# Performance work log

Measured on AMD Instinct MI355X. Metric: run time of the kernel, lower is better.

The kernel has to match this reference:

```python
import jax, jax.numpy as jnp
import numpy as np
from jax import lax

STRIDES = (4, 8, 16, 32, 64)
SIZES = (32, 64, 128, 256, 512)
RATIOS = (0.5, 1.0, 2.0)
IMG_H, IMG_W = 1024, 1024
PRE_NMS = 1000
POST_NMS = 1000
NMS_THRESH = 0.7
BBOX_CLIP = float(np.log(1000.0 / 16.0))
NEG_INF = -1e9


def _cell_anchors(size):
    a = []
    for r in RATIOS:
        w = size * np.sqrt(1.0 / r)
        h = size * np.sqrt(r)
        a.append([-w / 2.0, -h / 2.0, w / 2.0, h / 2.0])
    return np.array(a, np.float32)  # [A,4]


def _level_anchors(H, W, stride, size):
    cell = _cell_anchors(size)  # [A,4]
    ys = np.arange(H, dtype=np.float32) * stride
    xs = np.arange(W, dtype=np.float32) * stride
    yy, xx = np.meshgrid(ys, xs, indexing='ij')  # row-major (H,W)
    shifts = np.stack([xx, yy, xx, yy], axis=-1).reshape(-1, 1, 4)
    return jnp.asarray((shifts + cell[None]).reshape(-1, 4))  # [(H*W*A),4] in (H,W,A) order


def conv2d(x, w, b, pad):
    y = lax.conv_general_dilated(x, w, (1, 1), pad,
                                 dimension_numbers=('NCHW', 'OIHW', 'NCHW'))
    return y + b[None, :, None, None]


def decode(deltas, anchors):
    widths = anchors[:, 2] - anchors[:, 0] + 1.0
    heights = anchors[:, 3] - anchors[:, 1] + 1.0
    ctr_x = anchors[:, 0] + 0.5 * widths
    ctr_y = anchors[:, 1] + 0.5 * heights
    dx, dy = deltas[..., 0], deltas[..., 1]
    dw = jnp.minimum(deltas[..., 2], BBOX_CLIP)
    dh = jnp.minimum(deltas[..., 3], BBOX_CLIP)
    pcx = dx * widths + ctr_x
    pcy = dy * heights + ctr_y
    pw = jnp.exp(dw) * widths
    ph = jnp.exp(dh) * heights
    return jnp.stack([pcx - 0.5 * pw, pcy - 0.5 * ph,
                      pcx + 0.5 * pw - 1.0, pcy + 0.5 * ph - 1.0], axis=-1)


def iou_matrix(boxes):
    area = (boxes[:, 2] - boxes[:, 0]) * (boxes[:, 3] - boxes[:, 1])
    lt = jnp.maximum(boxes[:, None, :2], boxes[None, :, :2])
    rb = jnp.minimum(boxes[:, None, 2:], boxes[None, :, 2:])
    wh = jnp.maximum(rb - lt, 0.0)
    inter = wh[..., 0] * wh[..., 1]
    return inter / (area[:, None] + area[None, :] - inter + 1e-9)


def nms_keep(boxes):
    # boxes [N,4] already sorted by score desc; greedy NMS -> bool keep mask
    N = boxes.shape[0]
    iou = iou_matrix(boxes)

    def body(keep, i):
        row = jnp.take(iou, i, axis=0) > NMS_THRESH
        row = row.at[i].set(False)
        keep = jnp.where(keep[i], keep & ~row, keep)
        return keep, None

    keep, _ = lax.scan(body, jnp.ones((N,), bool), jnp.arange(N))
    return keep


def _forward(feats, conv_w, conv_b, cls_w, cls_b, bbox_w, bbox_b):
    level_boxes, level_scores = [], []
    for lvl, feat in enumerate(feats):
        B, _, H, W = feat.shape
        t = jax.nn.relu(conv2d(feat, conv_w, conv_b, 'SAME'))
        logits = conv2d(t, cls_w, cls_b, 'VALID')    # [B,A,H,W]
        breg = conv2d(t, bbox_w, bbox_b, 'VALID')    # [B,4A,H,W]
        A = logits.shape[1]
        scores = jnp.transpose(logits, (0, 2, 3, 1)).reshape(B, -1)            # (H,W,A)
        deltas = breg.reshape(B, A, 4, H, W).transpose(0, 3, 4, 1, 2).reshape(B, -1, 4)
        anchors = _level_anchors(H, W, STRIDES[lvl], SIZES[lvl])
        boxes = decode(deltas, anchors)  # [B,N,4]
        boxes = jnp.stack([jnp.clip(boxes[..., 0], 0.0, IMG_W - 1.0),
                           jnp.clip(boxes[..., 1], 0.0, IMG_H - 1.0),
                           jnp.clip(boxes[..., 2], 0.0, IMG_W - 1.0),
                           jnp.clip(boxes[..., 3], 0.0, IMG_H - 1.0)], axis=-1)
        k = min(PRE_NMS, scores.shape[1])
        top_s, idx = lax.top_k(scores, k)                                   # [B,k]
        top_b = jnp.take_along_axis(boxes, idx[..., None], axis=1)          # [B,k,4]
        keep = jax.vmap(nms_keep)(top_b)                                    # [B,k] bool
        level_scores.append(jnp.where(keep, top_s, NEG_INF))
        level_boxes.append(top_b)
    all_s = jnp.concatenate(level_scores, axis=1)
    all_b = jnp.concatenate(level_boxes, axis=1)
    fs, fi = lax.top_k(all_s, POST_NMS)                                     # [B,POST]
    fb = jnp.take_along_axis(all_b, fi[..., None], axis=1)                  # [B,POST,4]
    return jnp.concatenate([fb, fs[..., None]], axis=-1)                    # [B,POST,5]


def setup_inputs() -> dict:
    key = jax.random.key(0)
    ks = jax.random.split(key, 8)
    C = 256
    feats = {
        'feat0': jax.random.normal(ks[0], (2, C, 256, 256), jnp.float32),
        'feat1': jax.random.normal(ks[1], (2, C, 128, 128), jnp.float32),
        'feat2': jax.random.normal(ks[2], (2, C, 64, 64), jnp.float32),
        'feat3': jax.random.normal(ks[3], (2, C, 32, 32), jnp.float32),
        'feat4': jax.random.normal(ks[4], (2, C, 16, 16), jnp.float32),
    }
    params = {
        'conv_w': jax.random.normal(ks[5], (C, C, 3, 3), jnp.float32) * 0.01,
        'conv_b': jnp.zeros((C,), jnp.float32),
        'cls_w': jax.random.normal(ks[6], (3, C, 1, 1), jnp.float32) * 0.01,
        'cls_b': jnp.zeros((3,), jnp.float32),
        'bbox_w': jax.random.normal(ks[7], (12, C, 1, 1), jnp.float32) * 0.01,
        'bbox_b': jnp.zeros((12,), jnp.float32),
    }
    return {**feats, **params}


def reference(feat0, feat1, feat2, feat3, feat4, conv_w, conv_b, cls_w, cls_b, bbox_w, bbox_b):
    return _forward([feat0, feat1, feat2, feat3, feat4],
                    conv_w, conv_b, cls_w, cls_b, bbox_w, bbox_b)
```

## Files before the change

### kernel.cpp

```cpp
#include <hip/hip_runtime.h>
#include <cmath>


#define NTOT_PER_IMG 261888
#define ATOT_PER_IMG 4768

__constant__ int c_NLVL[5] = {196608, 49152, 12288, 3072, 768};
__constant__ int c_KLVL[5] = {1000, 1000, 1000, 1000, 768};
__constant__ int c_LOFF[5] = {0, 196608, 245760, 258048, 261120};
__constant__ int c_AOFF[5] = {0, 1000, 2000, 3000, 4000};

struct Anch { float cx1[3]; float cy1[3]; };
struct ConvCfg { Anch an[5]; };

__device__ __forceinline__ void ldsBarrier() {
  asm volatile("s_waitcnt lgkmcnt(0)" ::: "memory");
  __builtin_amdgcn_s_barrier();
  asm volatile("" ::: "memory");
}

__global__ __launch_bounds__(256) void wtrans(const float* __restrict__ Wsrc,
                                              float* __restrict__ Wt) {
  __shared__ float T[16][17];
  int k0 = blockIdx.x * 16;
  int o0 = blockIdx.y * 16;
  int i = threadIdx.x >> 4, j = threadIdx.x & 15;
  T[i][j] = Wsrc[(size_t)(o0 + i) * 2304 + (k0 + j)];
  __syncthreads();
  Wt[(size_t)(k0 + i) * 256 + (o0 + j)] = T[j][i];
}

__global__ __launch_bounds__(256, 2) void conv_gemm(
    const float* __restrict__ f0, const float* __restrict__ f1,
    const float* __restrict__ f2, const float* __restrict__ f3,
    const float* __restrict__ f4, const float* __restrict__ Wt,
    const float* __restrict__ convb, const float* __restrict__ clsw,
    const float* __restrict__ clsb, const float* __restrict__ bboxw,
    const float* __restrict__ bboxb, float* __restrict__ scoresOut,
    float4* __restrict__ boxesOut, ConvCfg cfg) {
  __shared__ __align__(16) float s_mem[5424];
  __shared__ float s_Red2[272];
  float* const s_w = s_mem;
  float* const s_x = s_mem + 4608;
  float* const s_tl = s_mem;

  int b = blockIdx.x;
  const float* feat;
  int lvl, img, tile, H, logW, stride, lvlOff;
  if (b < 2048) {
    lvl = 0; feat = f0; H = 256; logW = 8; stride = 4; lvlOff = 0;
    img = b >> 10; tile = b & 1023;
  } else if (b < 2560) {
    lvl = 1; feat = f1; H = 128; logW = 7; stride = 8; lvlOff = 196608;
    int r = b - 2048; img = r >> 8; tile = r & 255;
  } else if (b < 2688) {
    lvl = 2; feat = f2; H = 64; logW = 6; stride = 16; lvlOff = 245760;
    int r = b - 2560; img = r >> 6; tile = r & 63;
  } else if (b < 2720) {
    lvl = 3; feat = f3; H = 32; logW = 5; stride = 32; lvlOff = 258048;
    int r = b - 2688; img = r >> 4; tile = r & 15;
  } else {
    lvl = 4; feat = f4; H = 16; logW = 4; stride = 64; lvlOff = 261120;
    int r = b - 2720; img = r >> 2; tile = r & 3;
  }
  const int W = H, HW = H * W;
  const int p0 = tile * 64;
  const float* fimg = feat + (size_t)img * 256 * HW;

  const int log2nc = (logW < 6) ? logW : 6;
  const int ncols = 1 << log2nc;
  const int R = 64 >> log2nc;
  const int py0 = p0 >> logW;
  const int c_start = p0 & (W - 1);
  const int WIN = ncols + 2;
  const int NX = (R + 2) * WIN;

  const int tid = threadIdx.x;
  const int oc0 = (tid >> 3) * 8;
  const int pxg = tid & 7;
  const int px0 = pxg * 8;
  const int trow = px0 >> log2nc;
  const int tcol0 = px0 & (ncols - 1);

  int goffX = -1, loffX = -1;
  if (tid < NX) {
    int lr = tid / WIN;
    int lc = tid - lr * WIN;
    int sy = py0 - 1 + lr;
    int sx = c_start - 1 + lc;
    loffX = lr * 68 + lc;
    if (sy >= 0 && sy < H && sx >= 0 && sx < W) goffX = sy * W + sx;
  }

  float acc[8][8];
#pragma unroll
  for (int i = 0; i < 8; i++)
#pragma unroll
    for (int p = 0; p < 8; p++) acc[i][p] = 0.f;

  {
    const float4* wg = (const float4*)(Wt);
    float4* wl = (float4*)(s_w);
    wl[tid] = wg[tid];
    wl[tid + 256] = wg[tid + 256];
    if (tid < 64) wl[tid + 512] = wg[tid + 512];
    if (loffX >= 0) s_x[loffX] = (goffX >= 0) ? fimg[goffX] : 0.f;
  }
  ldsBarrier();

#pragma unroll 1
  for (int ic = 0; ic < 256; ic++) {
    const float* wb = s_w + (ic & 1) * 2304;
    const float* xb = s_x + (ic & 1) * 408;
    float* wn = s_w + ((ic + 1) & 1) * 2304;
    float* xn = s_x + ((ic + 1) & 1) * 408;

    float4 pw0, pw1, pw2;
    float pxv;
    if (ic < 255) {
      const float4* wg = (const float4*)(Wt + (size_t)(ic + 1) * 2304);
      pw0 = wg[tid];
      pw1 = wg[tid + 256];
      if (tid < 64) pw2 = wg[tid + 512];
      const float* fnext = fimg + (size_t)(ic + 1) * HW;
      pxv = (goffX >= 0) ? fnext[goffX] : 0.f;
    }

#pragma unroll
    for (int ky = 0; ky < 3; ky++) {
      const float* xr = xb + (trow + ky) * 68 + tcol0;
      float4 xA = *(const float4*)(xr);
      float4 xB = *(const float4*)(xr + 4);
      float2 xC = *(const float2*)(xr + 8);
      float xw[10] = {xA.x, xA.y, xA.z, xA.w,
                      xB.x, xB.y, xB.z, xB.w, xC.x, xC.y};
#pragma unroll
      for (int kx = 0; kx < 3; kx++) {
        const float* wr = wb + (ky * 3 + kx) * 256 + oc0;
        float4 wa = *(const float4*)(wr);
        float4 wc = *(const float4*)(wr + 4);
        float wv[8] = {wa.x, wa.y, wa.z, wa.w, wc.x, wc.y, wc.z, wc.w};
#pragma unroll
        for (int i = 0; i < 8; i++)
#pragma unroll
          for (int p = 0; p < 8; p++)
            acc[i][p] = __builtin_fmaf(wv[i], xw[p + kx], acc[i][p]);
      }
    }

    if (ic < 255) {
      float4* wl = (float4*)(wn);
      wl[tid] = pw0;
      wl[tid + 256] = pw1;
      if (tid < 64) wl[tid + 512] = pw2;
      if (loffX >= 0) xn[loffX] = pxv;
    }
    ldsBarrier();
  }

  float cb[8];
#pragma unroll
  for (int i = 0; i < 8; i++) cb[i] = convb[oc0 + i];

  const Anch an = cfg.an[lvl];
  const float BCLIP = (float)4.135166556742356;
  const size_t obase = (size_t)img * NTOT_PER_IMG + lvlOff;

#pragma unroll 1
  for (int r = 0; r < 4; r++) {
    if ((pxg >> 1) == r) {
      int pl = px0 - 16 * r;
#pragma unroll
      for (int p = 0; p < 8; p++) {
        float4 v0 = make_float4(fmaxf(acc[0][p] + cb[0], 0.f),
                                fmaxf(acc[1][p] + cb[1], 0.f),
                                fmaxf(acc[2][p] + cb[2], 0.f),
                                fmaxf(acc[3][p] + cb[3], 0.f));
        float4 v1 = make_float4(fmaxf(acc[4][p] + cb[4], 0.f),
                                fmaxf(acc[5][p] + cb[5], 0.f),
                                fmaxf(acc[6][p] + cb[6], 0.f),
                                fmaxf(acc[7][p] + cb[7], 0.f));
        *(float4*)(s_tl + (pl + p) * 256 + oc0) = v0;
        *(float4*)(s_tl + (pl + p) * 256 + oc0 + 4) = v1;
      }
    }
    __syncthreads();

    if (tid < 240) {
      int px = tid / 15, c = tid - px * 15;
      const float* wr0 = (c < 3) ? (clsw + c * 256) : (bboxw + (c - 3) * 256);
      float bb = (c < 3) ? clsb[c] : bboxb[c - 3];
      const float* trow2 = &s_tl[px * 256];
      float tot = 0.f;
#pragma unroll
      for (int g = 0; g < 16; g++) {
        const float* wr = wr0 + g * 16;
        const float* tr = trow2 + g * 16;
        float s = 0.f;
#pragma unroll
        for (int i = 0; i < 16; i++) s += wr[i] * tr[i];
        tot += s;
      }
      s_Red2[px * 17 + c] = tot + bb;
    }
    __syncthreads();

    if (tid < 48) {
      int px = tid / 3, a = tid - px * 3;
      int pxl = p0 + r * 16 + px;
      int gy = pxl >> logW, gx = pxl & (W - 1);
      float sc = s_Red2[px * 17 + a];
      float dxv = s_Red2[px * 17 + 3 + a * 4 + 0];
      float dyv = s_Red2[px * 17 + 3 + a * 4 + 1];
      float dwv = s_Red2[px * 17 + 3 + a * 4 + 2];
      float dhv = s_Red2[px * 17 + 3 + a * 4 + 3];
      float sx = (float)(gx * stride), sy = (float)(gy * stride);
      float x1 = __fadd_rn(sx, an.cx1[a]);
      float x2 = __fsub_rn(sx, an.cx1[a]);
      float y1 = __fadd_rn(sy, an.cy1[a]);
      float y2 = __fsub_rn(sy, an.cy1[a]);
      float wdt = __fadd_rn(__fsub_rn(x2, x1), 1.0f);
      float hgt = __fadd_rn(__fsub_rn(y2, y1), 1.0f);
      float ctx = __fadd_rn(x1, __fmul_rn(0.5f, wdt));
      float cty = __fadd_rn(y1, __fmul_rn(0.5f, hgt));
      float dw = fminf(dwv, BCLIP), dh = fminf(dhv, BCLIP);
      float pcx = __fadd_rn(__fmul_rn(dxv, wdt), ctx);
      float pcy = __fadd_rn(__fmul_rn(dyv, hgt), cty);
      float pw = __fmul_rn(expf(dw), wdt);
      float ph = __fmul_rn(expf(dh), hgt);
      float hw = __fmul_rn(0.5f, pw), hh = __fmul_rn(0.5f, ph);
      float bx1 = __fsub_rn(pcx, hw);
      float by1 = __fsub_rn(pcy, hh);
      float bx2 = __fsub_rn(__fadd_rn(pcx, hw), 1.0f);
      float by2 = __fsub_rn(__fadd_rn(pcy, hh), 1.0f);
      bx1 = fminf(fmaxf(bx1, 0.f), 1023.f);
      by1 = fminf(fmaxf(by1, 0.f), 1023.f);
      bx2 = fminf(fmaxf(bx2, 0.f), 1023.f);
      by2 = fminf(fmaxf(by2, 0.f), 1023.f);
      size_t o = obase + (size_t)pxl * 3 + a;
      scoresOut[o] = sc;
      boxesOut[o] = make_float4(bx1, by1, bx2, by2);
    }
    __syncthreads();
  }
}

__device__ __forceinline__ unsigned fkey(float f) {
  unsigned b = __float_as_uint(f);
  return (b & 0x80000000u) ? ~b : (b | 0x80000000u);
}
__device__ __forceinline__ float funkey(unsigned u) {
  unsigned b = (u & 0x80000000u) ? (u & 0x7fffffffu) : ~u;
  return __uint_as_float(b);
}

template <bool FINAL>
__global__ __launch_bounds__(1024) void topk_kernel(
    const float* __restrict__ scoresIn, const float4* __restrict__ boxesIn,
    float* __restrict__ scoresOut, float4* __restrict__ boxesOut,
    float* __restrict__ finalOut) {
  __shared__ unsigned long long keys[1024];
  __shared__ unsigned hist[256];
  __shared__ unsigned s_comm[4];
  int lvl = 0, img, N, k;
  const float* src;
  const float4* bsrc;
  if (FINAL) {
    img = blockIdx.x; N = ATOT_PER_IMG; k = 1000;
    src = scoresIn + (size_t)img * ATOT_PER_IMG;
    bsrc = boxesIn + (size_t)img * ATOT_PER_IMG;
  } else {
    lvl = blockIdx.x; img = blockIdx.y;
    N = c_NLVL[lvl]; k = c_KLVL[lvl];
    src = scoresIn + (size_t)img * NTOT_PER_IMG + c_LOFF[lvl];
    bsrc = boxesIn + (size_t)img * NTOT_PER_IMG + c_LOFF[lvl];
  }
  const int tid = threadIdx.x;

  unsigned pref = 0, pmask = 0, krem = (unsigned)k, cntT = 0;
  for (int pass = 3; pass >= 0; pass--) {
    int shift = pass * 8;
    if (tid < 256) hist[tid] = 0;
    __syncthreads();
    for (int i = tid; i < N; i += 1024) {
      unsigned u = fkey(src[i]);
      if ((u & pmask) == pref) atomicAdd(&hist[(u >> shift) & 255], 1u);
    }
    __syncthreads();
    if (tid == 0) {
      unsigned cum = 0;
      for (int d = 255; d >= 0; d--) {
        unsigned c = hist[d];
        if (cum + c >= krem) {
          s_comm[0] = krem - cum; s_comm[1] = c; s_comm[2] = (unsigned)d;
          break;
        }
        cum += c;
      }
    }
    __syncthreads();
    krem = s_comm[0]; cntT = s_comm[1];
    pref |= s_comm[2] << shift;
    pmask |= 0xFFu << shift;
    __syncthreads();
  }
  const unsigned T = pref, r = krem;
  unsigned m = (unsigned)N;
  if (r < cntT) {
    unsigned lo = 0, hi = (unsigned)N;
    while (lo < hi) {
      unsigned mid = (lo + hi) >> 1;
      if (tid == 0) s_comm[3] = 0;
      __syncthreads();
      for (unsigned i = tid; i < mid; i += 1024)
        if (fkey(src[i]) == T) atomicAdd(&s_comm[3], 1u);
      __syncthreads();
      unsigned c = s_comm[3];
      __syncthreads();
      if (c >= r) hi = mid; else lo = mid + 1;
    }
    m = lo;
  }
  if (tid == 0) s_comm[3] = 0;
  __syncthreads();
  for (int i = tid; i < N; i += 1024) {
    unsigned u = fkey(src[i]);
    if (u > T || (u == T && (unsigned)i < m)) {
      unsigned p = atomicAdd(&s_comm[3], 1u);
      if (p < 1024)
        keys[p] = ((unsigned long long)u << 32) | (unsigned)(~(unsigned)i);
    }
  }
  __syncthreads();
  if (tid >= k) keys[tid] = 0ull;
  __syncthreads();
  for (unsigned k2 = 2; k2 <= 1024; k2 <<= 1) {
    for (unsigned j = k2 >> 1; j > 0; j >>= 1) {
      unsigned i = tid, ixj = i ^ j;
      if (ixj > i) {
        unsigned long long a = keys[i], b = keys[ixj];
        bool sw = ((i & k2) == 0) ? (a < b) : (a > b);
        if (sw) { keys[i] = b; keys[ixj] = a; }
      }
      __syncthreads();
    }
  }
  if (tid < k) {
    unsigned long long key = keys[tid];
    unsigned u = (unsigned)(key >> 32);
    unsigned idx = ~((unsigned)key);
    float sc = funkey(u);
    float4 b = bsrc[idx];
    if (FINAL) {
      float* o = finalOut + ((size_t)img * 1000 + tid) * 5;
      o[0] = b.x; o[1] = b.y; o[2] = b.z; o[3] = b.w; o[4] = sc;
    } else {
      scoresOut[(size_t)img * ATOT_PER_IMG + c_AOFF[lvl] + tid] = sc;
      boxesOut[(size_t)img * ATOT_PER_IMG + c_AOFF[lvl] + tid] = b;
    }
  }
}

__global__ __launch_bounds__(256) void nms_matrix(
    const float4* __restrict__ allb, unsigned long long* __restrict__ supp) {
  int lvl = blockIdx.x, img = blockIdx.y, rb = blockIdx.z;
  int k = c_KLVL[lvl];
  int task = img * 5 + lvl;
  const float4* src = allb + (size_t)img * ATOT_PER_IMG + c_AOFF[lvl];
  __shared__ float4 bb[1000];
  __shared__ float ar[1000];
  for (int j = threadIdx.x; j < k; j += 256) {
    float4 b = src[j];
    bb[j] = b;
    ar[j] = __fmul_rn(__fsub_rn(b.z, b.x), __fsub_rn(b.w, b.y));
  }
  __syncthreads();
  int i = rb * 256 + threadIdx.x;
  if (i < k) {
    float4 bi = bb[i];
    float ai = ar[i];
    unsigned long long* row = supp + ((size_t)task * 1024 + i) * 16;
    int jw0 = i >> 6;
    for (int jw = 0; jw < jw0; jw++) row[jw] = 0ull;
    for (int jw = jw0; jw < 16; jw++) {
      unsigned long long bits = 0;
      int jbase = jw * 64;
      for (int jj = 0; jj < 64; jj++) {
        int j = jbase + jj;
        if (j > i && j < k) {
          float4 bj = bb[j];
          float ltx = fmaxf(bi.x, bj.x), lty = fmaxf(bi.y, bj.y);
          float rbx = fminf(bi.z, bj.z), rby = fminf(bi.w, bj.w);
          float wx = fmaxf(__fsub_rn(rbx, ltx), 0.f);
          float wy = fmaxf(__fsub_rn(rby, lty), 0.f);
          float inter = __fmul_rn(wx, wy);
          float den = __fadd_rn(__fsub_rn(__fadd_rn(ai, ar[j]), inter), 1e-9f);
          if (__fdiv_rn(inter, den) > 0.7f) bits |= 1ull << jj;
        }
      }
      row[jw] = bits;
    }
  }
}

__global__ __launch_bounds__(64) void nms_scan(
    const float* __restrict__ topS, const unsigned long long* __restrict__ supp,
    float* __restrict__ fscore) {
  int lvl = blockIdx.x, img = blockIdx.y;
  int k = c_KLVL[lvl];
  int task = img * 5 + lvl;
  int lane = threadIdx.x;
  const unsigned long long* base = supp + (size_t)task * 1024 * 16;
  unsigned long long rem = 0, keep = 0;
  for (int b0 = 0; b0 < k; b0 += 16) {
    unsigned long long buf[16];
#pragma unroll
    for (int t = 0; t < 16; t++) {
      int i = b0 + t;
      buf[t] = (lane < 16 && i < k) ? base[(size_t)i * 16 + lane] : 0ull;
    }
#pragma unroll
    for (int t = 0; t < 16; t++) {
      int i = b0 + t;
      if (i >= k) break;
      int wi = i >> 6, bi = i & 63;
      unsigned long long rw = __shfl(rem, wi);
      if (!((rw >> bi) & 1ull)) {
        rem |= buf[t];
        if (lane == wi) keep |= (1ull << bi);
      }
    }
  }
  const float* ts = topS + (size_t)img * ATOT_PER_IMG + c_AOFF[lvl];
  float* fs = fscore + (size_t)img * ATOT_PER_IMG + c_AOFF[lvl];
  for (int i = lane; i < k; i += 64) {
    int wi = i >> 6;
    unsigned long long kw = __shfl(keep, wi);
    fs[i] = ((kw >> (i & 63)) & 1ull) ? ts[i] : -1e9f;
  }
}

static Anch mkAnch(double size) {
  Anch a;
  const double R[3] = {0.5, 1.0, 2.0};
  for (int i = 0; i < 3; i++) {
    double w = size * sqrt(1.0 / R[i]);
    double h = size * sqrt(R[i]);
    a.cx1[i] = (float)(-w / 2.0);
    a.cy1[i] = (float)(-h / 2.0);
  }
  return a;
}

extern "C" void kernel_launch(void* const* d_in, const int* in_sizes, int n_in,
                              void* d_out, int out_size, void* d_ws,
                              size_t ws_size, hipStream_t stream) {
  (void)in_sizes; (void)n_in; (void)out_size; (void)ws_size;
  const float* f0 = (const float*)d_in[0];
  const float* f1 = (const float*)d_in[1];
  const float* f2 = (const float*)d_in[2];
  const float* f3 = (const float*)d_in[3];
  const float* f4 = (const float*)d_in[4];
  const float* conv_w = (const float*)d_in[5];
  const float* conv_b = (const float*)d_in[6];
  const float* cls_w  = (const float*)d_in[7];
  const float* cls_b  = (const float*)d_in[8];
  const float* bbox_w = (const float*)d_in[9];
  const float* bbox_b = (const float*)d_in[10];
  float* out = (float*)d_out;

  float* wsf = (float*)d_ws;
  float* Wt     = wsf;
  float* scores = Wt + 589824;
  float* boxes  = scores + 2 * NTOT_PER_IMG;
  float* topS   = boxes + (size_t)2 * NTOT_PER_IMG * 4;
  float* allb   = topS + 2 * ATOT_PER_IMG;
  float* fscore = allb + (size_t)2 * ATOT_PER_IMG * 4;
  unsigned long long* supp =
      (unsigned long long*)(fscore + 2 * ATOT_PER_IMG);

  wtrans<<<dim3(144, 16), 256, 0, stream>>>(conv_w, Wt);

  ConvCfg cfg;
  const double SZ[5] = {32, 64, 128, 256, 512};
  for (int l = 0; l < 5; l++) cfg.an[l] = mkAnch(SZ[l]);

  conv_gemm<<<2728, 256, 0, stream>>>(f0, f1, f2, f3, f4, Wt, conv_b, cls_w,
                                      cls_b, bbox_w, bbox_b, scores,
                                      (float4*)boxes, cfg);

  topk_kernel<false><<<dim3(5, 2), 1024, 0, stream>>>(
      scores, (const float4*)boxes, topS, (float4*)allb, nullptr);
  nms_matrix<<<dim3(5, 2, 4), 256, 0, stream>>>((const float4*)allb, supp);
  nms_scan<<<dim3(5, 2), 64, 0, stream>>>(topS, supp, fscore);
  topk_kernel<true><<<2, 1024, 0, stream>>>(
      fscore, (const float4*)allb, nullptr, nullptr, out);
}
```

Before: 3.552 ms.

## Load conv weights directly into LDS with global_load_lds and raise occupancy

Replaces the register-staged weight prefetch (global load to float4 registers, then LDS store) with direct global-to-LDS DMA loads of 16 bytes per lane. This frees the prefetch registers, and launch bounds are raised from 2 to 3 blocks per CU. The custom lgkmcnt-only barrier is replaced by __syncthreads, which also waits on vmcnt so the async LDS writes are complete before use. The gain depends on whether 16-byte global_load_lds is supported and the per-lane address pattern is correct, and the higher occupancy target may cause register spills in the 64-accumulator loop.

```diff
diff --git a/kernel.cpp b/kernel.cpp
--- a/kernel.cpp
+++ b/kernel.cpp
@@ -13,10 +13,10 @@
 struct Anch { float cx1[3]; float cy1[3]; };
 struct ConvCfg { Anch an[5]; };
 
-__device__ __forceinline__ void ldsBarrier() {
-  asm volatile("s_waitcnt lgkmcnt(0)" ::: "memory");
-  __builtin_amdgcn_s_barrier();
-  asm volatile("" ::: "memory");
+__device__ __forceinline__ void gl16(const float* g, float* l) {
+  __builtin_amdgcn_global_load_lds(
+      (const __attribute__((address_space(1))) void*)g,
+      (__attribute__((address_space(3))) void*)l, 16, 0, 0);
 }
 
 __global__ __launch_bounds__(256) void wtrans(const float* __restrict__ Wsrc,
@@ -30,7 +30,7 @@
   Wt[(size_t)(k0 + i) * 256 + (o0 + j)] = T[j][i];
 }
 
-__global__ __launch_bounds__(256, 2) void conv_gemm(
+__global__ __launch_bounds__(256, 3) void conv_gemm(
     const float* __restrict__ f0, const float* __restrict__ f1,
     const float* __restrict__ f2, const float* __restrict__ f3,
     const float* __restrict__ f4, const float* __restrict__ Wt,
@@ -98,30 +98,28 @@
 #pragma unroll
     for (int p = 0; p < 8; p++) acc[i][p] = 0.f;
 
+  const int t4 = tid << 2;
+
   {
-    const float4* wg = (const float4*)(Wt);
-    float4* wl = (float4*)(s_w);
-    wl[tid] = wg[tid];
-    wl[tid + 256] = wg[tid + 256];
-    if (tid < 64) wl[tid + 512] = wg[tid + 512];
+    gl16(Wt + t4, s_w + t4);
+    gl16(Wt + 1024 + t4, s_w + 1024 + t4);
+    if (tid < 64) gl16(Wt + 2048 + t4, s_w + 2048 + t4);
     if (loffX >= 0) s_x[loffX] = (goffX >= 0) ? fimg[goffX] : 0.f;
   }
-  ldsBarrier();
+  __syncthreads();
 
 #pragma unroll 1
   for (int ic = 0; ic < 256; ic++) {
     const float* wb = s_w + (ic & 1) * 2304;
     const float* xb = s_x + (ic & 1) * 408;
-    float* wn = s_w + ((ic + 1) & 1) * 2304;
-    float* xn = s_x + ((ic + 1) & 1) * 408;
-
-    float4 pw0, pw1, pw2;
+
     float pxv;
     if (ic < 255) {
-      const float4* wg = (const float4*)(Wt + (size_t)(ic + 1) * 2304);
-      pw0 = wg[tid];
-      pw1 = wg[tid + 256];
-      if (tid < 64) pw2 = wg[tid + 512];
+      const float* wg = Wt + (size_t)(ic + 1) * 2304;
+      float* wn = s_w + ((ic + 1) & 1) * 2304;
+      gl16(wg + t4, wn + t4);
+      gl16(wg + 1024 + t4, wn + 1024 + t4);
+      if (tid < 64) gl16(wg + 2048 + t4, wn + 2048 + t4);
       const float* fnext = fimg + (size_t)(ic + 1) * HW;
       pxv = (goffX >= 0) ? fnext[goffX] : 0.f;
     }
@@ -149,13 +147,10 @@
     }
 
     if (ic < 255) {
-      float4* wl = (float4*)(wn);
-      wl[tid] = pw0;
-      wl[tid + 256] = pw1;
-      if (tid < 64) wl[tid + 512] = pw2;
+      float* xn = s_x + ((ic + 1) & 1) * 408;
       if (loffX >= 0) xn[loffX] = pxv;
     }
-    ldsBarrier();
+    __syncthreads();
   }
 
   float cb[8];
```

Result: slower. 6.550 ms (+84.4%).
